# Optimization experiments

Hardware: AMD Instinct MI355X
Metric: run time of the kernel (lower is better)

## Reference

```python
import jax, jax.numpy as jnp
import numpy as np

NUM_HEADS = 4
NUM_GROUPS = 32
EPS = 1e-5


def group_norm(x, gamma, beta):
    B, C, H, W = x.shape
    g = x.reshape(B, NUM_GROUPS, C // NUM_GROUPS, H, W)
    mean = g.mean(axis=(2, 3, 4), keepdims=True)
    var = g.var(axis=(2, 3, 4), keepdims=True)
    g = (g - mean) * jax.lax.rsqrt(var + EPS)
    x = g.reshape(B, C, H, W)
    return x * gamma[None, :, None, None] + beta[None, :, None, None]


def setup_inputs() -> dict:
    key = jax.random.key(0)
    ks = jax.random.split(key, 7)
    B, C, H, W = 16, 256, 32, 32
    x = jax.random.normal(ks[0], (B, C, H, W), dtype=jnp.float32)
    gn_gamma = jnp.ones((C,), dtype=jnp.float32)
    gn_beta = jnp.zeros((C,), dtype=jnp.float32)
    s = 1.0 / np.sqrt(C)
    qkv_w = jax.random.normal(ks[1], (3 * C, C), dtype=jnp.float32) * s
    qkv_b = jnp.zeros((3 * C,), dtype=jnp.float32)
    proj_w = jax.random.normal(ks[2], (C, C), dtype=jnp.float32) * s
    proj_b = jnp.zeros((C,), dtype=jnp.float32)
    return {"x": x, "gn_gamma": gn_gamma, "gn_beta": gn_beta,
            "qkv_w": qkv_w, "qkv_b": qkv_b, "proj_w": proj_w, "proj_b": proj_b}


def reference(x, gn_gamma, gn_beta, qkv_w, qkv_b, proj_w, proj_b):
    B, C, H, W = x.shape
    nh = NUM_HEADS
    d = C // nh
    N = H * W

    h = group_norm(x, gn_gamma, gn_beta)
    # 1x1 conv == channel matmul
    qkv = jnp.einsum('bchw,oc->bohw', h, qkv_w) + qkv_b[None, :, None, None]
    qkv = qkv.reshape(B, 3, nh, d, N)
    q, k, v = qkv[:, 0], qkv[:, 1], qkv[:, 2]  # each [B, nh, d, N]

    scale = 1.0 / jnp.sqrt(jnp.asarray(d, dtype=x.dtype))
    attn = jnp.einsum('bhdn,bhdm->bhnm', q, k) * scale  # [B, nh, N, N]
    attn = jax.nn.softmax(attn, axis=-1)
    out = jnp.einsum('bhnm,bhdm->bhdn', attn, v)  # [B, nh, d, N]
    out = out.reshape(B, C, H, W)

    out = jnp.einsum('bchw,oc->bohw', out, proj_w) + proj_b[None, :, None, None]
    return x + out
```

## Files before the change

kernel.cpp:

```cpp
#include <hip/hip_runtime.h>
#include <math.h>

typedef unsigned short u16;
typedef unsigned int u32;
typedef __attribute__((ext_vector_type(8))) short s16x8;
typedef __attribute__((ext_vector_type(4))) float f32x4;

#define NB 16
#define NN 1024
#define GN_EPS 1e-5f

static __device__ __forceinline__ u16 f2bf(float f) {
    union { float f; u32 u; } v; v.f = f;
    return (u16)((v.u + 0x8000u) >> 16);
}
static __device__ __forceinline__ u32 pk2(float a, float b) {
    union { float f; u32 u; } A, B; A.f = a; B.f = b;
    return __builtin_amdgcn_perm(A.u + 0x8000u, B.u + 0x8000u, 0x03020706u);
}
static __device__ __forceinline__ u32 cvtpk2(float a, float b) {
    u32 r;
    asm("v_cvt_pk_bf16_f32 %0, %1, %2" : "=v"(r) : "v"(a), "v"(b));
    return r;
}

#define GLL16(gp, lp) __builtin_amdgcn_global_load_lds( \
    (const __attribute__((address_space(1))) void*)(const void*)(gp), \
    (__attribute__((address_space(3))) void*)(void*)(lp), 16, 0, 0)

__global__ __launch_bounds__(256) void gn_stats_kernel(
    const float* __restrict__ x, float2* __restrict__ stats)
{
    const int bg = blockIdx.x;
    const int t  = threadIdx.x;
    const float4* xb = (const float4*)(x + (size_t)bg * 8192);
    float s = 0.f, ss = 0.f;
#pragma unroll
    for (int i = 0; i < 8; ++i) {
        float4 f = xb[t + i * 256];
        s  += f.x + f.y + f.z + f.w;
        ss += f.x * f.x + f.y * f.y + f.z * f.z + f.w * f.w;
    }
#pragma unroll
    for (int off = 32; off > 0; off >>= 1) {
        s  += __shfl_down(s, off);
        ss += __shfl_down(ss, off);
    }
    __shared__ float red[8];
    const int wid = t >> 6;
    if ((t & 63) == 0) { red[wid] = s; red[4 + wid] = ss; }
    __syncthreads();
    if (t == 0) {
        float sa = red[0] + red[1] + red[2] + red[3];
        float sb = red[4] + red[5] + red[6] + red[7];
        float mean = sa * (1.0f / 8192.0f);
        float var  = sb * (1.0f / 8192.0f) - mean * mean;
        stats[bg] = make_float2(mean, 1.0f / sqrtf(var + GN_EPS));
    }
}

__global__ __launch_bounds__(256) void wcvt_kernel(
    const float* __restrict__ qkv_w, const float* __restrict__ proj_w,
    u16* __restrict__ wqb, u16* __restrict__ wpb)
{
    int i = blockIdx.x * 256 + threadIdx.x;
    if (i < 49152) {
        float4 f = ((const float4*)qkv_w)[i];
        *(uint2*)(wqb + (size_t)i * 4) = make_uint2(pk2(f.x, f.y), pk2(f.z, f.w));
    } else {
        int j = i - 49152;
        float4 f = ((const float4*)proj_w)[j];
        *(uint2*)(wpb + (size_t)j * 4) = make_uint2(pk2(f.x, f.y), pk2(f.z, f.w));
    }
}

__global__ __launch_bounds__(256) void gnorm_t_kernel(
    const float* __restrict__ x, const float2* __restrict__ stats,
    const float* __restrict__ gamma, const float* __restrict__ beta,
    u16* __restrict__ Xt)
{
    const int b = blockIdx.z, ct = blockIdx.y, nt = blockIdx.x;
    const int t = threadIdx.x;
    __shared__ float T[64][65];
    const float* xb = x + ((size_t)b * 256 + ct * 64) * NN + nt * 64;
#pragma unroll
    for (int i = 0; i < 4; ++i) {
        int row = i * 16 + (t >> 4), col = (t & 15) * 4;
        int ch = ct * 64 + row;
        float2 st = stats[b * 32 + (ch >> 3)];
        float gmv = st.y * gamma[ch];
        float btv = beta[ch] - st.x * gmv;
        float4 f = *(const float4*)&xb[(size_t)row * NN + col];
        T[row][col + 0] = f.x * gmv + btv;
        T[row][col + 1] = f.y * gmv + btv;
        T[row][col + 2] = f.z * gmv + btv;
        T[row][col + 3] = f.w * gmv + btv;
    }
    __syncthreads();
    u16* dst = Xt + ((size_t)b * NN + nt * 64) * 256 + ct * 64;
#pragma unroll
    for (int p = 0; p < 2; ++p) {
        int idx = t + p * 256;
        int nl = idx >> 3, c8 = idx & 7;
        s16x8 pv;
#pragma unroll
        for (int j = 0; j < 8; ++j) pv[j] = (short)f2bf(T[c8 * 8 + j][nl]);
        *(s16x8*)(dst + (size_t)nl * 256 + c8 * 8) = pv;
    }
}

__global__ __launch_bounds__(256) void qkv_mfma_kernel(
    const u16* __restrict__ Wb, const float* __restrict__ bias,
    const u16* __restrict__ Xt,
    u16* __restrict__ qh, u16* __restrict__ kh, u16* __restrict__ vh)
{
    const int b = blockIdx.z, ot = blockIdx.y, nt = blockIdx.x;
    const int t = threadIdx.x, w = t >> 6, l = t & 63;
    const int g = l >> 4, c = l & 15;
    __shared__ u16 Slds[32 * 512];
    const u16* Xb = Xt + ((size_t)b * NN + nt * 128) * 256;
    const u16* Wo = Wb + (size_t)ot * 64 * 256;
    const int part = ot >> 2, h = ot & 3;
    const size_t bhoff = (size_t)(b * 4 + h) << 16;

    if (part < 2) {
#pragma unroll
        for (int s = w; s < 32; s += 4) {
            int osub = s >> 3, ks = s & 7;
            GLL16(Wo + (size_t)(osub * 16 + c) * 256 + ks * 32 + g * 8, Slds + s * 512);
        }
        s16x8 a0[8], a1[8];
#pragma unroll
        for (int ks = 0; ks < 8; ++ks) {
            a0[ks] = *(const s16x8*)(Xb + (size_t)((2 * w) * 16 + c) * 256 + ks * 32 + g * 8);
            a1[ks] = *(const s16x8*)(Xb + (size_t)((2 * w + 1) * 16 + c) * 256 + ks * 32 + g * 8);
        }
        f32x4 acc[2][4];
#pragma unroll
        for (int i = 0; i < 2; ++i)
#pragma unroll
            for (int j = 0; j < 4; ++j) acc[i][j] = (f32x4){0.f, 0.f, 0.f, 0.f};
        __syncthreads();
#pragma unroll
        for (int ks = 0; ks < 8; ++ks)
#pragma unroll
            for (int j = 0; j < 4; ++j) {
                s16x8 bf = *(const s16x8*)(Slds + (j * 8 + ks) * 512 + l * 8);
                acc[0][j] = __builtin_amdgcn_mfma_f32_16x16x32_bf16(a0[ks], bf, acc[0][j], 0, 0, 0);
                acc[1][j] = __builtin_amdgcn_mfma_f32_16x16x32_bf16(a1[ks], bf, acc[1][j], 0, 0, 0);
            }
        const float sc = (part == 0) ? 0.125f * 1.44269504088896f : 1.0f;
        float bv[4];
#pragma unroll
        for (int j = 0; j < 4; ++j) bv[j] = bias[ot * 64 + j * 16 + c];
        u16* dst = (part == 0 ? qh : kh) + bhoff + (size_t)(nt * 128) * 64;
#pragma unroll
        for (int i = 0; i < 2; ++i)
#pragma unroll
            for (int j = 0; j < 4; ++j)
#pragma unroll
                for (int r = 0; r < 4; ++r) {
                    int n = (2 * w + i) * 16 + g * 4 + r;
                    dst[(size_t)n * 64 + j * 16 + c] = f2bf((acc[i][j][r] + bv[j]) * sc);
                }
    } else {
        f32x4 acc[8];
#pragma unroll
        for (int j = 0; j < 8; ++j) acc[j] = (f32x4){0.f, 0.f, 0.f, 0.f};
        for (int kk = 0; kk < 256; kk += 128) {
            if (kk) __syncthreads();
#pragma unroll
            for (int s = w; s < 32; s += 4) {
                int nsub = s >> 2, ks = s & 3;
                GLL16(Xb + (size_t)(nsub * 16 + c) * 256 + kk + ks * 32 + g * 8, Slds + s * 512);
            }
            __syncthreads();
#pragma unroll
            for (int ks = 0; ks < 4; ++ks) {
                s16x8 a = *(const s16x8*)(Wo + (size_t)(w * 16 + c) * 256 + kk + ks * 32 + g * 8);
#pragma unroll
                for (int j = 0; j < 8; ++j) {
                    s16x8 xf = *(const s16x8*)(Slds + (j * 4 + ks) * 512 + l * 8);
                    acc[j] = __builtin_amdgcn_mfma_f32_16x16x32_bf16(a, xf, acc[j], 0, 0, 0);
                }
            }
        }
        float bv[4];
#pragma unroll
        for (int r = 0; r < 4; ++r) bv[r] = bias[ot * 64 + w * 16 + g * 4 + r];
        u16* dst = vh + bhoff;
#pragma unroll
        for (int j = 0; j < 8; ++j)
#pragma unroll
            for (int r = 0; r < 4; ++r) {
                int d = w * 16 + g * 4 + r;
                int m = nt * 128 + j * 16 + c;
                dst[(size_t)d * NN + m] = f2bf(acc[j][r] + bv[r]);
            }
    }
}

__global__ __launch_bounds__(512, 4) void attn_mfma_kernel(
    const u16* __restrict__ qh, const u16* __restrict__ kh,
    const u16* __restrict__ vh, u16* __restrict__ aoT)
{
    const int t = threadIdx.x;
    const int w = t >> 6, l = t & 63;
    const int g = l >> 4, c = l & 15;
    const int bid = blockIdx.x;
    const int xcd = bid & 7;
    const int idx = bid >> 3;
    const int qt  = idx & 7;
    const int grp = (idx >> 3) * 8 + xcd;
    const int b = grp >> 2, h = grp & 3;
    const size_t bhoff = (size_t)grp << 16;
    const int n_base = qt * 128 + w * 16;

    __shared__ u16 Klds[4][8 * 512];
    __shared__ u16 Vlds[4][8 * 512];
    __shared__ u16 Plds[8][2 * 512];

    const u16* qb = qh + bhoff;
    const u16* kb = kh + bhoff;
    const u16* vb = vh + bhoff;

    const int msub = w >> 1, uu = w & 1;

    s16x8 qf[2];
#pragma unroll
    for (int u = 0; u < 2; ++u)
        qf[u] = *(const s16x8*)(qb + (size_t)(n_base + c) * 64 + u * 32 + g * 8);

    s16x8 onef;
#pragma unroll
    for (int j = 0; j < 8; ++j) onef[j] = (short)0x3F80;

    f32x4 Oacc[4];
    f32x4 Lacc = (f32x4){0.f, 0.f, 0.f, 0.f};
#pragma unroll
    for (int ds = 0; ds < 4; ++ds) Oacc[ds] = (f32x4){0.f, 0.f, 0.f, 0.f};

    u16* pw = &Plds[w][0];

#define STK(tt) GLL16(kb + (size_t)((tt) * 64 + msub * 16 + c) * 64 + uu * 32 + g * 8, &Klds[(tt) & 3][w * 512])
#define STV(tt) GLL16(vb + (size_t)(msub * 16 + c) * NN + (tt) * 64 + uu * 32 + g * 8, &Vlds[(tt) & 3][w * 512])

    auto tile = [&](int buf) {
        const u16* Kc = &Klds[buf][0];
        const u16* Vc = &Vlds[buf][0];
        f32x4 S[4];
#pragma unroll
        for (int ms = 0; ms < 4; ++ms) S[ms] = (f32x4){0.f, 0.f, 0.f, 0.f};
#pragma unroll
        for (int ms = 0; ms < 4; ++ms)
#pragma unroll
            for (int u = 0; u < 2; ++u) {
                s16x8 af = *(const s16x8*)(Kc + (ms * 2 + u) * 512 + l * 8);
                S[ms] = __builtin_amdgcn_mfma_f32_16x16x32_bf16(af, qf[u], S[ms], 0, 0, 0);
            }
        s16x8 vf[4][2];
#pragma unroll
        for (int ds = 0; ds < 4; ++ds)
#pragma unroll
            for (int u = 0; u < 2; ++u)
                vf[ds][u] = *(const s16x8*)(Vc + (ds * 2 + u) * 512 + l * 8);
#pragma unroll
        for (int ms = 0; ms < 4; ++ms)
#pragma unroll
            for (int r = 0; r < 4; ++r) S[ms][r] = __builtin_amdgcn_exp2f(S[ms][r]);
#pragma unroll
        for (int ms = 0; ms < 4; ++ms) {
            u32 d0 = cvtpk2(S[ms][0], S[ms][1]);
            u32 d1 = cvtpk2(S[ms][2], S[ms][3]);
            int off = (ms >> 1) * 512 + ((ms & 1) * 2 + (g >> 1)) * 128 + c * 8 + (g & 1) * 4;
            *(uint2*)(pw + off) = make_uint2(d0, d1);
        }
#pragma unroll
        for (int u = 0; u < 2; ++u) {
            s16x8 pf = *(const s16x8*)(pw + u * 512 + l * 8);
#pragma unroll
            for (int ds = 0; ds < 4; ++ds)
                Oacc[ds] = __builtin_amdgcn_mfma_f32_16x16x32_bf16(vf[ds][u], pf, Oacc[ds], 0, 0, 0);
            Lacc = __builtin_amdgcn_mfma_f32_16x16x32_bf16(onef, pf, Lacc, 0, 0, 0);
        }
    };

    STK(0); STV(0); STK(1); STV(1);

    for (int it = 0; it < 8; ++it) {
        if (it < 7) {
            STK(2 * it + 2); STV(2 * it + 2);
            STK(2 * it + 3); STV(2 * it + 3);
            asm volatile("s_waitcnt vmcnt(4)" ::: "memory");
        } else {
            asm volatile("s_waitcnt vmcnt(0)" ::: "memory");
        }
        __builtin_amdgcn_s_barrier();
        asm volatile("" ::: "memory");

        tile((2 * it) & 3);
        tile((2 * it + 1) & 3);

        asm volatile("" ::: "memory");
        __builtin_amdgcn_s_barrier();
    }

    u16* aob = aoT + (size_t)b * NN * 256 + h * 64;
    float inv = 1.0f / Lacc[0];
    const size_t nrow = (size_t)(n_base + c) * 256;
#pragma unroll
    for (int ds = 0; ds < 4; ++ds) {
        u32 lo = cvtpk2(Oacc[ds][0] * inv, Oacc[ds][1] * inv);
        u32 hi = cvtpk2(Oacc[ds][2] * inv, Oacc[ds][3] * inv);
        *(uint2*)(aob + nrow + ds * 16 + g * 4) = make_uint2(lo, hi);
    }
#undef STK
#undef STV
}

__global__ __launch_bounds__(256) void proj_mfma_kernel(
    const u16* __restrict__ Wb, const float* __restrict__ bias,
    const u16* __restrict__ aoT, const float* __restrict__ x,
    float* __restrict__ out)
{
    const int b = blockIdx.z, ot = blockIdx.y, nt = blockIdx.x;
    const int t = threadIdx.x, w = t >> 6, l = t & 63;
    const int g = l >> 4, c = l & 15;
    __shared__ u16 Slds[32 * 512];
    const u16* Xb = aoT + ((size_t)b * NN + nt * 128) * 256;
    const u16* Wo = Wb + (size_t)ot * 64 * 256;

    f32x4 acc[8];
#pragma unroll
    for (int j = 0; j < 8; ++j) acc[j] = (f32x4){0.f, 0.f, 0.f, 0.f};
    for (int kk = 0; kk < 256; kk += 128) {
        if (kk) __syncthreads();
#pragma unroll
        for (int s = w; s < 32; s += 4) {
            int nsub = s >> 2, ks = s & 3;
            GLL16(Xb + (size_t)(nsub * 16 + c) * 256 + kk + ks * 32 + g * 8, Slds + s * 512);
        }
        __syncthreads();
#pragma unroll
        for (int ks = 0; ks < 4; ++ks) {
            s16x8 a = *(const s16x8*)(Wo + (size_t)(w * 16 + c) * 256 + kk + ks * 32 + g * 8);
#pragma unroll
            for (int j = 0; j < 8; ++j) {
                s16x8 xf = *(const s16x8*)(Slds + (j * 4 + ks) * 512 + l * 8);
                acc[j] = __builtin_amdgcn_mfma_f32_16x16x32_bf16(a, xf, acc[j], 0, 0, 0);
            }
        }
    }
    float bv[4];
#pragma unroll
    for (int r = 0; r < 4; ++r) bv[r] = bias[ot * 64 + w * 16 + g * 4 + r];
#pragma unroll
    for (int j = 0; j < 8; ++j)
#pragma unroll
        for (int r = 0; r < 4; ++r) {
            int o = ot * 64 + w * 16 + g * 4 + r;
            int n = nt * 128 + j * 16 + c;
            size_t addr = ((size_t)b * 256 + o) * NN + n;
            out[addr] = acc[j][r] + bv[r] + x[addr];
        }
}

extern "C" void kernel_launch(void* const* d_in, const int* in_sizes, int n_in,
                              void* d_out, int out_size, void* d_ws, size_t ws_size,
                              hipStream_t stream)
{
    const float* x      = (const float*)d_in[0];
    const float* gamma  = (const float*)d_in[1];
    const float* beta   = (const float*)d_in[2];
    const float* qkv_w  = (const float*)d_in[3];
    const float* qkv_b  = (const float*)d_in[4];
    const float* proj_w = (const float*)d_in[5];
    const float* proj_b = (const float*)d_in[6];
    float* out = (float*)d_out;

    float* ws = (float*)d_ws;
    float2* stats = (float2*)ws;
    u16* Xt  = (u16*)(ws + 1024);
    u16* wqb = Xt + (size_t)4194304;
    u16* wpb = wqb + (size_t)196608;
    u16* qh  = wpb + (size_t)65536;
    u16* kh  = qh + (size_t)4194304;
    u16* vh  = kh + (size_t)4194304;
    u16* aoT = vh + (size_t)4194304;

    gn_stats_kernel<<<dim3(NB * 32), 256, 0, stream>>>(x, stats);
    wcvt_kernel<<<dim3(256), 256, 0, stream>>>(qkv_w, proj_w, wqb, wpb);
    gnorm_t_kernel<<<dim3(16, 4, NB), 256, 0, stream>>>(x, stats, gamma, beta, Xt);

    qkv_mfma_kernel<<<dim3(8, 12, NB), 256, 0, stream>>>(
        wqb, qkv_b, Xt, qh, kh, vh);

    attn_mfma_kernel<<<dim3(512), 512, 0, stream>>>(qh, kh, vh, aoT);

    proj_mfma_kernel<<<dim3(8, 4, NB), 256, 0, stream>>>(
        wpb, proj_b, aoT, x, out);
}
```

Baseline: 83.33 us.

## Fuse Q and K projections per block and add MFMA priority hints in attention

```diff
diff --git a/kernel.cpp b/kernel.cpp
--- a/kernel.cpp
+++ b/kernel.cpp
@@ -109,7 +109,7 @@
     }
 }
 
-__global__ __launch_bounds__(256) void qkv_mfma_kernel(
+__global__ __launch_bounds__(256, 4) void qkv_mfma_kernel(
     const u16* __restrict__ Wb, const float* __restrict__ bias,
     const u16* __restrict__ Xt,
     u16* __restrict__ qh, u16* __restrict__ kh, u16* __restrict__ vh)
@@ -119,15 +119,17 @@
     const int g = l >> 4, c = l & 15;
     __shared__ u16 Slds[32 * 512];
     const u16* Xb = Xt + ((size_t)b * NN + nt * 128) * 256;
-    const u16* Wo = Wb + (size_t)ot * 64 * 256;
-    const int part = ot >> 2, h = ot & 3;
-    const size_t bhoff = (size_t)(b * 4 + h) << 16;
-
-    if (part < 2) {
+
+    if (ot < 4) {
+        const int h = ot;
+        const size_t bhoff = (size_t)(b * 4 + h) << 16;
+        const u16* Wq = Wb + (size_t)(h)     * 64 * 256;
+        const u16* Wk = Wb + (size_t)(4 + h) * 64 * 256;
+
 #pragma unroll
         for (int s = w; s < 32; s += 4) {
             int osub = s >> 3, ks = s & 7;
-            GLL16(Wo + (size_t)(osub * 16 + c) * 256 + ks * 32 + g * 8, Slds + s * 512);
+            GLL16(Wq + (size_t)(osub * 16 + c) * 256 + ks * 32 + g * 8, Slds + s * 512);
         }
         s16x8 a0[8], a1[8];
 #pragma unroll
@@ -149,21 +151,63 @@
                 acc[0][j] = __builtin_amdgcn_mfma_f32_16x16x32_bf16(a0[ks], bf, acc[0][j], 0, 0, 0);
                 acc[1][j] = __builtin_amdgcn_mfma_f32_16x16x32_bf16(a1[ks], bf, acc[1][j], 0, 0, 0);
             }
-        const float sc = (part == 0) ? 0.125f * 1.44269504088896f : 1.0f;
-        float bv[4];
-#pragma unroll
-        for (int j = 0; j < 4; ++j) bv[j] = bias[ot * 64 + j * 16 + c];
-        u16* dst = (part == 0 ? qh : kh) + bhoff + (size_t)(nt * 128) * 64;
+        __syncthreads();
+
+#pragma unroll
+        for (int s = w; s < 32; s += 4) {
+            int osub = s >> 3, ks = s & 7;
+            GLL16(Wk + (size_t)(osub * 16 + c) * 256 + ks * 32 + g * 8, Slds + s * 512);
+        }
+        {
+            const float sc = 0.125f * 1.44269504088896f;
+            float bv[4];
+#pragma unroll
+            for (int j = 0; j < 4; ++j) bv[j] = bias[h * 64 + j * 16 + c];
+            u16* dst = qh + bhoff + (size_t)(nt * 128) * 64;
+#pragma unroll
+            for (int i = 0; i < 2; ++i)
+#pragma unroll
+                for (int j = 0; j < 4; ++j)
+#pragma unroll
+                    for (int r = 0; r < 4; ++r) {
+                        int n = (2 * w + i) * 16 + g * 4 + r;
+                        dst[(size_t)n * 64 + j * 16 + c] = f2bf((acc[i][j][r] + bv[j]) * sc);
+                    }
+        }
 #pragma unroll
         for (int i = 0; i < 2; ++i)
 #pragma unroll
-            for (int j = 0; j < 4; ++j)
-#pragma unroll
-                for (int r = 0; r < 4; ++r) {
-                    int n = (2 * w + i) * 16 + g * 4 + r;
-                    dst[(size_t)n * 64 + j * 16 + c] = f2bf((acc[i][j][r] + bv[j]) * sc);
-                }
+            for (int j = 0; j < 4; ++j) acc[i][j] = (f32x4){0.f, 0.f, 0.f, 0.f};
+        asm volatile("s_waitcnt vmcnt(32)" ::: "memory");
+        __builtin_amdgcn_s_barrier();
+        asm volatile("" ::: "memory");
+#pragma unroll
+        for (int ks = 0; ks < 8; ++ks)
+#pragma unroll
+            for (int j = 0; j < 4; ++j) {
+                s16x8 bf = *(const s16x8*)(Slds + (j * 8 + ks) * 512 + l * 8);
+                acc[0][j] = __builtin_amdgcn_mfma_f32_16x16x32_bf16(a0[ks], bf, acc[0][j], 0, 0, 0);
+                acc[1][j] = __builtin_amdgcn_mfma_f32_16x16x32_bf16(a1[ks], bf, acc[1][j], 0, 0, 0);
+            }
+        {
+            float bv[4];
+#pragma unroll
+            for (int j = 0; j < 4; ++j) bv[j] = bias[(4 + h) * 64 + j * 16 + c];
+            u16* dst = kh + bhoff + (size_t)(nt * 128) * 64;
+#pragma unroll
+            for (int i = 0; i < 2; ++i)
+#pragma unroll
+                for (int j = 0; j < 4; ++j)
+#pragma unroll
+                    for (int r = 0; r < 4; ++r) {
+                        int n = (2 * w + i) * 16 + g * 4 + r;
+                        dst[(size_t)n * 64 + j * 16 + c] = f2bf(acc[i][j][r] + bv[j]);
+                    }
+        }
     } else {
+        const int h = ot - 4;
+        const size_t bhoff = (size_t)(b * 4 + h) << 16;
+        const u16* Wo = Wb + (size_t)(8 + h) * 64 * 256;
         f32x4 acc[8];
 #pragma unroll
         for (int j = 0; j < 8; ++j) acc[j] = (f32x4){0.f, 0.f, 0.f, 0.f};
@@ -187,7 +231,7 @@
         }
         float bv[4];
 #pragma unroll
-        for (int r = 0; r < 4; ++r) bv[r] = bias[ot * 64 + w * 16 + g * 4 + r];
+        for (int r = 0; r < 4; ++r) bv[r] = bias[(8 + h) * 64 + w * 16 + g * 4 + r];
         u16* dst = vh + bhoff;
 #pragma unroll
         for (int j = 0; j < 8; ++j)
@@ -251,6 +295,7 @@
         f32x4 S[4];
 #pragma unroll
         for (int ms = 0; ms < 4; ++ms) S[ms] = (f32x4){0.f, 0.f, 0.f, 0.f};
+        __builtin_amdgcn_s_setprio(1);
 #pragma unroll
         for (int ms = 0; ms < 4; ++ms)
 #pragma unroll
@@ -258,6 +303,7 @@
                 s16x8 af = *(const s16x8*)(Kc + (ms * 2 + u) * 512 + l * 8);
                 S[ms] = __builtin_amdgcn_mfma_f32_16x16x32_bf16(af, qf[u], S[ms], 0, 0, 0);
             }
+        __builtin_amdgcn_s_setprio(0);
         s16x8 vf[4][2];
 #pragma unroll
         for (int ds = 0; ds < 4; ++ds)
@@ -275,6 +321,7 @@
             int off = (ms >> 1) * 512 + ((ms & 1) * 2 + (g >> 1)) * 128 + c * 8 + (g & 1) * 4;
             *(uint2*)(pw + off) = make_uint2(d0, d1);
         }
+        __builtin_amdgcn_s_setprio(1);
 #pragma unroll
         for (int u = 0; u < 2; ++u) {
             s16x8 pf = *(const s16x8*)(pw + u * 512 + l * 8);
@@ -283,6 +330,7 @@
                 Oacc[ds] = __builtin_amdgcn_mfma_f32_16x16x32_bf16(vf[ds][u], pf, Oacc[ds], 0, 0, 0);
             Lacc = __builtin_amdgcn_mfma_f32_16x16x32_bf16(onef, pf, Lacc, 0, 0, 0);
         }
+        __builtin_amdgcn_s_setprio(0);
     };
 
     STK(0); STV(0); STK(1); STV(1);
@@ -392,7 +440,7 @@
     wcvt_kernel<<<dim3(256), 256, 0, stream>>>(qkv_w, proj_w, wqb, wpb);
     gnorm_t_kernel<<<dim3(16, 4, NB), 256, 0, stream>>>(x, stats, gamma, beta, Xt);
 
-    qkv_mfma_kernel<<<dim3(8, 12, NB), 256, 0, stream>>>(
+    qkv_mfma_kernel<<<dim3(8, 8, NB), 256, 0, stream>>>(
         wqb, qkv_b, Xt, qh, kh, vh);
 
     attn_mfma_kernel<<<dim3(512), 512, 0, stream>>>(qh, kh, vh, aoT);
```

Measured after the change: 80.90 us. 1.03x faster.
